# Kernel optimization log

Measured on AMD Instinct MI355X. Metric: run time of the kernel, lower is better.

Reference implementation:

```python
import jax, jax.numpy as jnp
import numpy as np

N = 10000
E = 160000
IN_CH = 128
HID = 128
HEADS = 4
OUT_CH = 1  # forced by nn.Linear(heads, 1) applied after conv2


def _linear_params(key, out_f, in_f):
    k1, k2 = jax.random.split(key)
    bound = 1.0 / np.sqrt(in_f)
    W = jax.random.uniform(k1, (out_f, in_f), jnp.float32, -bound, bound)
    b = jax.random.uniform(k2, (out_f,), jnp.float32, -bound, bound)
    return W, b


def setup_inputs() -> dict:
    key = jax.random.key(0)
    ks = jax.random.split(key, 12)
    x = jax.random.normal(ks[0], (N, IN_CH), jnp.float32)
    edge_index = jax.random.randint(ks[1], (2, E), 0, N, jnp.int64)

    # conv1: TransformerConv(IN_CH, HID, HEADS)
    Wq1, bq1 = _linear_params(ks[2], HEADS * HID, IN_CH)
    Wk1, bk1 = _linear_params(ks[3], HEADS * HID, IN_CH)
    Wv1, bv1 = _linear_params(ks[4], HEADS * HID, IN_CH)
    Ws1, bs1 = _linear_params(ks[5], HEADS * HID, IN_CH)  # root/skip

    # conv2: TransformerConv(HID*HEADS, OUT_CH, HEADS)
    d2 = HID * HEADS
    Wq2, bq2 = _linear_params(ks[6], HEADS * OUT_CH, d2)
    Wk2, bk2 = _linear_params(ks[7], HEADS * OUT_CH, d2)
    Wv2, bv2 = _linear_params(ks[8], HEADS * OUT_CH, d2)
    Ws2, bs2 = _linear_params(ks[9], HEADS * OUT_CH, d2)

    # final nn.Linear(HEADS, 1)
    Wl, bl = _linear_params(ks[10], 1, HEADS)

    return dict(x=x, edge_index=edge_index,
                Wq1=Wq1, bq1=bq1, Wk1=Wk1, bk1=bk1, Wv1=Wv1, bv1=bv1, Ws1=Ws1, bs1=bs1,
                Wq2=Wq2, bq2=bq2, Wk2=Wk2, bk2=bk2, Wv2=Wv2, bv2=bv2, Ws2=Ws2, bs2=bs2,
                Wl=Wl, bl=bl)


def transformer_conv(x, edge_index, Wq, bq, Wk, bk, Wv, bv, Ws, bs, heads, ch):
    # PyG TransformerConv defaults: concat=True, root_weight=True, beta=False
    n = x.shape[0]
    q = (x @ Wq.T + bq).reshape(n, heads, ch)
    k = (x @ Wk.T + bk).reshape(n, heads, ch)
    v = (x @ Wv.T + bv).reshape(n, heads, ch)

    src, dst = edge_index[0], edge_index[1]  # messages flow src -> dst
    # per-edge attention logits [E, H]
    logits = jnp.einsum('ehc,ehc->eh', q[dst], k[src]) / np.sqrt(ch).astype(np.float32)

    # segment softmax over edges grouped by destination node
    seg_max = jax.ops.segment_max(logits, dst, num_segments=n)  # [N, H]
    seg_max = jnp.where(jnp.isfinite(seg_max), seg_max, 0.0)
    ex = jnp.exp(logits - seg_max[dst])
    denom = jax.ops.segment_sum(ex, dst, num_segments=n)  # [N, H]
    alpha = ex / jnp.maximum(denom[dst], 1e-16)  # [E, H]

    # scatter-aggregate weighted values
    msgs = alpha[:, :, None] * v[src]  # [E, H, C]
    out = jax.ops.segment_sum(msgs, dst, num_segments=n)  # [N, H, C]
    out = out.reshape(n, heads * ch)
    # root/skip connection
    return out + (x @ Ws.T + bs)


def reference(x, edge_index,
              Wq1, bq1, Wk1, bk1, Wv1, bv1, Ws1, bs1,
              Wq2, bq2, Wk2, bk2, Wv2, bv2, Ws2, bs2,
              Wl, bl):
    h = transformer_conv(x, edge_index, Wq1, bq1, Wk1, bk1, Wv1, bv1, Ws1, bs1, HEADS, HID)
    h = jax.nn.relu(h)
    # dropout is identity in eval mode
    h = transformer_conv(h, edge_index, Wq2, bq2, Wk2, bk2, Wv2, bv2, Ws2, bs2, HEADS, OUT_CH)
    h = h @ Wl.T + bl  # [N, 1]
    return jnp.mean(h, axis=0, keepdims=True)  # [1, 1]
```

## Files before the change

kernel.cpp:

```cpp
#include <hip/hip_runtime.h>
#include <math.h>

#define NN 10000
#define NE 160000
#define NROWT 79
#define NGEMM (NROWT * 32)

typedef __attribute__((ext_vector_type(8))) short bf16x8;
typedef __attribute__((ext_vector_type(4))) float f32x4;
typedef __attribute__((ext_vector_type(2))) float f32x2;

#if defined(__has_builtin)
#if __has_builtin(__builtin_amdgcn_cvt_pk_fp8_f32) && __has_builtin(__builtin_amdgcn_cvt_pk_f32_fp8)
#define HW_FP8 1
#endif
#endif

__device__ inline ushort f2bf(float x) {
  uint u = __float_as_uint(x);
  return (ushort)((u + 0x7fffu + ((u >> 16) & 1u)) >> 16);
}

__device__ inline void unpack8(uint4 u, float* f) {
  f[0] = __uint_as_float(u.x << 16); f[1] = __uint_as_float(u.x & 0xffff0000u);
  f[2] = __uint_as_float(u.y << 16); f[3] = __uint_as_float(u.y & 0xffff0000u);
  f[4] = __uint_as_float(u.z << 16); f[5] = __uint_as_float(u.z & 0xffff0000u);
  f[6] = __uint_as_float(u.w << 16); f[7] = __uint_as_float(u.w & 0xffff0000u);
}

#ifndef HW_FP8
__device__ inline float fp8_dec1(uint b) {
  uint s = b >> 7, e = (b >> 3) & 15, m = b & 7;
  float v = (e == 0) ? ldexpf((float)m, -9) : ldexpf((float)(8 + m), (int)e - 10);
  return s ? -v : v;
}
__device__ inline uint fp8_enc1(float x) {
  uint s = (__float_as_uint(x) >> 31) << 7;
  float a = fabsf(x);
  if (!(a < 448.f)) return s | 0x7e;
  if (a < 9.765625e-4f) return s;
  int e; float m = frexpf(a, &e);
  int E = e - 1, q;
  if (E < -6) {
    q = (int)rintf(ldexpf(a, 9));
    if (q == 0) return s;
    if (q >= 8) return s | 8;
    return s | (uint)q;
  }
  q = (int)rintf(ldexpf(m, 4));
  if (q == 16) { q = 8; ++E; }
  if (E > 8 || (E == 8 && q == 15)) return s | 0x7e;
  return s | ((uint)(E + 7) << 3) | (uint)(q - 8);
}
#endif

__device__ inline uint pack4_fp8(float a, float b, float c, float d) {
#ifdef HW_FP8
  uint w = (uint)__builtin_amdgcn_cvt_pk_fp8_f32(a, b, 0, false);
  w = (uint)__builtin_amdgcn_cvt_pk_fp8_f32(c, d, (int)w, true);
  return w;
#else
  return fp8_enc1(a) | (fp8_enc1(b) << 8) | (fp8_enc1(c) << 16) | (fp8_enc1(d) << 24);
#endif
}

__device__ inline void dec8_fp8(uint2 u, float* f) {
#ifdef HW_FP8
  f32x2 p0 = __builtin_amdgcn_cvt_pk_f32_fp8((int)u.x, false);
  f32x2 p1 = __builtin_amdgcn_cvt_pk_f32_fp8((int)u.x, true);
  f32x2 p2 = __builtin_amdgcn_cvt_pk_f32_fp8((int)u.y, false);
  f32x2 p3 = __builtin_amdgcn_cvt_pk_f32_fp8((int)u.y, true);
  f[0] = p0.x; f[1] = p0.y; f[2] = p1.x; f[3] = p1.y;
  f[4] = p2.x; f[5] = p2.y; f[6] = p3.x; f[7] = p3.y;
#else
  f[0] = fp8_dec1(u.x & 255); f[1] = fp8_dec1((u.x >> 8) & 255);
  f[2] = fp8_dec1((u.x >> 16) & 255); f[3] = fp8_dec1(u.x >> 24);
  f[4] = fp8_dec1(u.y & 255); f[5] = fp8_dec1((u.y >> 8) & 255);
  f[6] = fp8_dec1((u.y >> 16) & 255); f[7] = fp8_dec1(u.y >> 24);
#endif
}

__global__ __launch_bounds__(256) void prep_k(
    const float* __restrict__ x,
    const float* __restrict__ Wq1, const float* __restrict__ Wk1,
    const float* __restrict__ Wv1, const float* __restrict__ Ws1,
    ushort* __restrict__ x_bf, ushort* __restrict__ w1bf,
    const int* __restrict__ dst, int* __restrict__ deg)
{
  int i = blockIdx.x * 256 + threadIdx.x;
  if (i < NE) atomicAdd(&deg[dst[i]], 1);
  const int n4x = NN * 32;
  const int n4w = 512 * 128 / 4;
  if (i < n4x) {
    float4 v = ((const float4*)x)[i];
    ushort4 o;
    o.x = f2bf(v.x); o.y = f2bf(v.y); o.z = f2bf(v.z); o.w = f2bf(v.w);
    ((ushort4*)x_bf)[i] = o;
  } else {
    int c = i - n4x;
    if (c < 4 * n4w) {
      int seg = c >> 14, k = c & 16383;
      const float* W = (seg == 0) ? Wq1 : (seg == 1) ? Wk1
                     : (seg == 2) ? Wv1 : Ws1;
      float4 v = ((const float4*)W)[k];
      ushort4 o;
      o.x = f2bf(v.x); o.y = f2bf(v.y); o.z = f2bf(v.z); o.w = f2bf(v.w);
      ((ushort4*)(w1bf + ((size_t)seg << 16)))[k] = o;
    }
  }
}

__global__ __launch_bounds__(1024) void scan_k(
    const int* __restrict__ deg, int* __restrict__ rowptr,
    int* __restrict__ cursor)
{
  __shared__ int part[1024];
  int tid = threadIdx.x;
  int base = tid * 10;
  int loc[10]; int s = 0;
  #pragma unroll
  for (int i = 0; i < 10; ++i) {
    int v = (base + i < NN) ? deg[base + i] : 0;
    loc[i] = s; s += v;
  }
  part[tid] = s;
  __syncthreads();
  for (int off = 1; off < 1024; off <<= 1) {
    int v = (tid >= off) ? part[tid - off] : 0;
    __syncthreads();
    part[tid] += v;
    __syncthreads();
  }
  int prev = (tid == 0) ? 0 : part[tid - 1];
  #pragma unroll
  for (int i = 0; i < 10; ++i) {
    int idx = base + i;
    if (idx < NN) { int r = prev + loc[i]; rowptr[idx] = r; cursor[idx] = r; }
  }
  if (tid == 1023) rowptr[NN] = part[1023];
}

__global__ __launch_bounds__(256) void gemm_scatter(
    const ushort* __restrict__ xbf, const ushort* __restrict__ wbf,
    const float* __restrict__ bq, const float* __restrict__ bk,
    const float* __restrict__ bv, const float* __restrict__ bs,
    ushort* __restrict__ qbf, unsigned char* __restrict__ k8,
    unsigned char* __restrict__ v8, float* __restrict__ h1,
    const int* __restrict__ src, const int* __restrict__ dst,
    int* __restrict__ cursor, int* __restrict__ csr_src)
{
  if (blockIdx.x >= NGEMM) {
    int e = (blockIdx.x - NGEMM) * 256 + threadIdx.x;
    if (e < NE) {
      int pos = atomicAdd(&cursor[dst[e]], 1);
      csr_src[pos] = src[e];
    }
    return;
  }
  __shared__ __align__(16) ushort Al[128 * 128];
  __shared__ __align__(16) ushort Bl[64 * 128];
  const int row0 = (blockIdx.x % NROWT) << 7;
  const int ncol0 = (blockIdx.x / NROWT) << 6;
  const int tid = threadIdx.x;

  #pragma unroll
  for (int i = 0; i < 8; ++i) {
    int slot = tid + (i << 8);
    int r = slot >> 4, c = slot & 15;
    int gr = row0 + r;
    uint4 v = make_uint4(0u, 0u, 0u, 0u);
    if (gr < NN) v = *(const uint4*)(xbf + (size_t)gr * 128 + (c << 3));
    *(uint4*)(Al + r * 128 + ((c ^ (r & 7)) << 3)) = v;
  }
  #pragma unroll
  for (int i = 0; i < 4; ++i) {
    int slot = tid + (i << 8);
    int r = slot >> 4, c = slot & 15;
    uint4 v = *(const uint4*)(wbf + (size_t)(ncol0 + r) * 128 + (c << 3));
    *(uint4*)(Bl + r * 128 + ((c ^ (r & 7)) << 3)) = v;
  }
  __syncthreads();

  const int wid = tid >> 6, lane = tid & 63;
  const int wm = wid >> 1, wn = wid & 1;
  const int lr = lane & 15, lkg = lane >> 4;
  const int seg = ncol0 >> 9;
  const int colInSeg = ncol0 & 511;
  const bool swp = (seg == 1) || (seg == 2);

  f32x4 acc[4][2];
  #pragma unroll
  for (int m = 0; m < 4; ++m)
    #pragma unroll
    for (int n = 0; n < 2; ++n) acc[m][n] = (f32x4){0.f, 0.f, 0.f, 0.f};

  #pragma unroll
  for (int ks = 0; ks < 4; ++ks) {
    int c16 = (ks << 2) + lkg;
    bf16x8 a[4], b[2];
    #pragma unroll
    for (int mf = 0; mf < 4; ++mf) {
      int r = (wm << 6) + (mf << 4) + lr;
      a[mf] = *(const bf16x8*)(Al + r * 128 + ((c16 ^ (r & 7)) << 3));
    }
    #pragma unroll
    for (int nf = 0; nf < 2; ++nf) {
      int r = (wn << 5) + (nf << 4) + lr;
      b[nf] = *(const bf16x8*)(Bl + r * 128 + ((c16 ^ (r & 7)) << 3));
    }
    if (swp) {
      #pragma unroll
      for (int mf = 0; mf < 4; ++mf)
        #pragma unroll
        for (int nf = 0; nf < 2; ++nf)
          acc[mf][nf] = __builtin_amdgcn_mfma_f32_16x16x32_bf16(
              b[nf], a[mf], acc[mf][nf], 0, 0, 0);
    } else {
      #pragma unroll
      for (int mf = 0; mf < 4; ++mf)
        #pragma unroll
        for (int nf = 0; nf < 2; ++nf)
          acc[mf][nf] = __builtin_amdgcn_mfma_f32_16x16x32_bf16(
              a[mf], b[nf], acc[mf][nf], 0, 0, 0);
    }
  }

  const float* bias = (seg == 0) ? bq : (seg == 1) ? bk : (seg == 2) ? bv : bs;
  if (swp) {
    unsigned char* out8 = (seg == 1) ? k8 : v8;
    #pragma unroll
    for (int mf = 0; mf < 4; ++mf) {
      int xrow = row0 + (wm << 6) + (mf << 4) + lr;
      if (xrow >= NN) continue;
      #pragma unroll
      for (int nf = 0; nf < 2; ++nf) {
        int ch = colInSeg + (wn << 5) + (nf << 4) + (lkg << 2);
        float4 bb = *(const float4*)(bias + ch);
        uint w = pack4_fp8(acc[mf][nf][0] + bb.x, acc[mf][nf][1] + bb.y,
                           acc[mf][nf][2] + bb.z, acc[mf][nf][3] + bb.w);
        *(uint*)(out8 + (size_t)xrow * 512 + ch) = w;
      }
    }
  } else {
    #pragma unroll
    for (int mf = 0; mf < 4; ++mf) {
      #pragma unroll
      for (int nf = 0; nf < 2; ++nf) {
        int col = colInSeg + (wn << 5) + (nf << 4) + lr;
        float bb = bias[col];
        #pragma unroll
        for (int r = 0; r < 4; ++r) {
          int row = row0 + (wm << 6) + (mf << 4) + (lkg << 2) + r;
          if (row >= NN) continue;
          float val = acc[mf][nf][r] + bb;
          if (seg == 0) qbf[(size_t)row * 512 + col] = f2bf(val);
          else          h1[(size_t)row * 512 + col] = val;
        }
      }
    }
  }
}

#define EDGE8(ku, vu)                                                      \
  {                                                                        \
    float kf[8], vf[8];                                                    \
    dec8_fp8(ku, kf); dec8_fp8(vu, vf);                                    \
    float t = q[0]*kf[0] + q[1]*kf[1] + q[2]*kf[2] + q[3]*kf[3]            \
            + q[4]*kf[4] + q[5]*kf[5] + q[6]*kf[6] + q[7]*kf[7];           \
    t += __shfl_xor(t, 1);                                                 \
    t += __shfl_xor(t, 2);                                                 \
    t += __shfl_xor(t, 4);                                                 \
    t += __shfl_xor(t, 8);                                                 \
    float ex = __expf(t);                                                  \
    den += ex;                                                             \
    _Pragma("unroll")                                                      \
    for (int i = 0; i < 8; ++i) acc[i] += ex * vf[i];                      \
  }

__global__ __launch_bounds__(256) void attn1(
    const ushort* __restrict__ qbf, const unsigned char* __restrict__ k8,
    const unsigned char* __restrict__ v8, const int* __restrict__ rowptr,
    const int* __restrict__ csr_src, float* __restrict__ h1)
{
  __shared__ float part[2][64][9];
  int slot = threadIdx.x >> 7;
  int sub = (threadIdx.x >> 6) & 1;
  int n = blockIdx.x * 2 + slot;
  int lane = threadIdx.x & 63;
  int h = lane >> 4, c0 = (lane & 15) << 3;
  const int off = h * 128 + c0;
  float q[8];
  unpack8(*(const uint4*)(qbf + (size_t)n * 512 + off), q);
  #pragma unroll
  for (int i = 0; i < 8; ++i) q[i] *= 0.08838834764831845f;
  float acc[8] = {};
  float den = 0.f;
  int j = rowptr[n] + sub * 2, e1 = rowptr[n + 1];
  for (; j + 1 < e1; j += 4) {
    int s0 = csr_src[j], s1 = csr_src[j + 1];
    uint2 ka = *(const uint2*)(k8 + (size_t)s0 * 512 + off);
    uint2 va = *(const uint2*)(v8 + (size_t)s0 * 512 + off);
    uint2 kb = *(const uint2*)(k8 + (size_t)s1 * 512 + off);
    uint2 vb = *(const uint2*)(v8 + (size_t)s1 * 512 + off);
    EDGE8(ka, va)
    EDGE8(kb, vb)
  }
  if (j < e1) {
    int s0 = csr_src[j];
    uint2 ka = *(const uint2*)(k8 + (size_t)s0 * 512 + off);
    uint2 va = *(const uint2*)(v8 + (size_t)s0 * 512 + off);
    EDGE8(ka, va)
  }
  if (sub == 1) {
    #pragma unroll
    for (int i = 0; i < 8; ++i) part[slot][lane][i] = acc[i];
    part[slot][lane][8] = den;
  }
  __syncthreads();
  if (sub == 0) {
    #pragma unroll
    for (int i = 0; i < 8; ++i) acc[i] += part[slot][lane][i];
    den += part[slot][lane][8];
    float inv = 1.f / fmaxf(den, 1e-16f);
    float* op = h1 + (size_t)n * 512 + off;
    float4 s0 = *(const float4*)op, s1 = *(const float4*)(op + 4);
    float4 o0, o1;
    o0.x = fmaxf(s0.x + acc[0] * inv, 0.f);
    o0.y = fmaxf(s0.y + acc[1] * inv, 0.f);
    o0.z = fmaxf(s0.z + acc[2] * inv, 0.f);
    o0.w = fmaxf(s0.w + acc[3] * inv, 0.f);
    o1.x = fmaxf(s1.x + acc[4] * inv, 0.f);
    o1.y = fmaxf(s1.y + acc[5] * inv, 0.f);
    o1.z = fmaxf(s1.z + acc[6] * inv, 0.f);
    o1.w = fmaxf(s1.w + acc[7] * inv, 0.f);
    *(float4*)op = o0;
    *(float4*)(op + 4) = o1;
  }
}

__global__ __launch_bounds__(256) void gemm_l2(
    const float* __restrict__ h1,
    const float* __restrict__ Wq, const float* __restrict__ bq,
    const float* __restrict__ Wk, const float* __restrict__ bk,
    const float* __restrict__ Wv, const float* __restrict__ bv,
    const float* __restrict__ Ws, const float* __restrict__ bs,
    float* __restrict__ qkv2, float* __restrict__ acc2)
{
  __shared__ float red[4][64][17];
  int n0 = blockIdx.x * 64;
  int wid = threadIdx.x >> 6, lane = threadIdx.x & 63;
  int n = n0 + lane;
  const float* Wm[4] = {Wq, Wk, Wv, Ws};
  float s[16] = {};
  if (n < NN) {
    const float* a = h1 + (size_t)n * 512 + wid * 128;
    #pragma unroll 4
    for (int i = 0; i < 128; i += 4) {
      float4 av = *(const float4*)(a + i);
      #pragma unroll
      for (int j = 0; j < 16; ++j) {
        const float* w = Wm[j >> 2] + (size_t)(j & 3) * 512 + wid * 128 + i;
        s[j] += av.x * w[0] + av.y * w[1] + av.z * w[2] + av.w * w[3];
      }
    }
  }
  #pragma unroll
  for (int j = 0; j < 16; ++j) red[wid][lane][j] = s[j];
  __syncthreads();
  #pragma unroll
  for (int q = 0; q < 4; ++q) {
    int idx = threadIdx.x * 4 + q;
    int ln = idx >> 4, j = idx & 15;
    int nn2 = n0 + ln;
    if (nn2 >= NN) continue;
    float v = red[0][ln][j] + red[1][ln][j] + red[2][ln][j] + red[3][ln][j];
    int sg = j >> 2, r = j & 3;
    const float* bb = (sg == 0) ? bq : (sg == 1) ? bk : (sg == 2) ? bv : bs;
    v += bb[r];
    if (sg < 3) qkv2[nn2 * 12 + sg * 4 + r] = v;
    else        acc2[nn2 * 4 + r] = v;
  }
}

__global__ __launch_bounds__(256) void attn2(
    const float* __restrict__ qkv2, const int* __restrict__ rowptr,
    const int* __restrict__ csr_src, float* __restrict__ acc2)
{
  int t = blockIdx.x * 256 + threadIdx.x;
  if (t >= NN * 16) return;
  int n = t >> 4, h = (t >> 2) & 3, part = t & 3;
  float q = qkv2[n * 12 + h];
  float den = 0.f, acc = 0.f;
  int e1 = rowptr[n + 1];
  for (int j = rowptr[n] + part; j < e1; j += 4) {
    int s = csr_src[j];
    float k = qkv2[s * 12 + 4 + h];
    float v = qkv2[s * 12 + 8 + h];
    float ex = __expf(q * k);
    den += ex; acc += ex * v;
  }
  den += __shfl_xor(den, 1); acc += __shfl_xor(acc, 1);
  den += __shfl_xor(den, 2); acc += __shfl_xor(acc, 2);
  if (part == 0) acc2[n * 4 + h] += acc / fmaxf(den, 1e-16f);
}

__global__ __launch_bounds__(1024) void final_k(
    const float* __restrict__ acc2, const float* __restrict__ Wl,
    const float* __restrict__ bl, float* __restrict__ out)
{
  __shared__ float red[1024];
  float w0 = Wl[0], w1 = Wl[1], w2 = Wl[2], w3 = Wl[3];
  float s = 0.f;
  for (int n = threadIdx.x; n < NN; n += 1024) {
    float4 a = ((const float4*)acc2)[n];
    s += a.x * w0 + a.y * w1 + a.z * w2 + a.w * w3;
  }
  red[threadIdx.x] = s;
  __syncthreads();
  for (int off = 512; off; off >>= 1) {
    if (threadIdx.x < off) red[threadIdx.x] += red[threadIdx.x + off];
    __syncthreads();
  }
  if (threadIdx.x == 0) out[0] = bl[0] + red[0] * (1.0f / NN);
}

extern "C" void kernel_launch(void* const* d_in, const int* in_sizes, int n_in,
                              void* d_out, int out_size, void* d_ws, size_t ws_size,
                              hipStream_t stream)
{
  const float* x   = (const float*)d_in[0];
  const int*   ei  = (const int*)d_in[1];
  const float *Wq1 = (const float*)d_in[2],  *bq1 = (const float*)d_in[3];
  const float *Wk1 = (const float*)d_in[4],  *bk1 = (const float*)d_in[5];
  const float *Wv1 = (const float*)d_in[6],  *bv1 = (const float*)d_in[7];
  const float *Ws1 = (const float*)d_in[8],  *bs1 = (const float*)d_in[9];
  const float *Wq2 = (const float*)d_in[10], *bq2 = (const float*)d_in[11];
  const float *Wk2 = (const float*)d_in[12], *bk2 = (const float*)d_in[13];
  const float *Wv2 = (const float*)d_in[14], *bv2 = (const float*)d_in[15];
  const float *Ws2 = (const float*)d_in[16], *bs2 = (const float*)d_in[17];
  const float *Wl  = (const float*)d_in[18], *bl  = (const float*)d_in[19];
  const int* srcp = ei;
  const int* dstp = ei + NE;

  ushort* qbf  = (ushort*)d_ws;
  ushort* x_bf = qbf + (size_t)NN * 512;
  ushort* w1bf = x_bf + (size_t)NN * 128;
  unsigned char* k8 = (unsigned char*)(w1bf + (size_t)2048 * 128);
  unsigned char* v8 = k8 + (size_t)NN * 512;
  float*  h1   = (float*)(v8 + (size_t)NN * 512);
  float*  qkv2 = h1 + (size_t)NN * 512;
  float*  acc2 = qkv2 + (size_t)NN * 12;
  int*   deg     = (int*)(acc2 + (size_t)NN * 4);
  int*   rowptr  = deg + NN;
  int*   cursor  = rowptr + NN + 1;
  int*   csr_src = cursor + NN;

  hipMemsetAsync(deg, 0, (size_t)NN * sizeof(int), stream);
  {
    const int total = NN * 32 + 4 * (512 * 128 / 4);
    prep_k<<<(total + 255) / 256, 256, 0, stream>>>(
        x, Wq1, Wk1, Wv1, Ws1, x_bf, w1bf, dstp, deg);
  }
  scan_k<<<1, 1024, 0, stream>>>(deg, rowptr, cursor);

  gemm_scatter<<<NGEMM + (NE + 255) / 256, 256, 0, stream>>>(
      x_bf, w1bf, bq1, bk1, bv1, bs1, qbf, k8, v8, h1,
      srcp, dstp, cursor, csr_src);

  attn1<<<NN / 2, 256, 0, stream>>>(qbf, k8, v8, rowptr, csr_src, h1);
  gemm_l2<<<(NN + 63) / 64, 256, 0, stream>>>(
      h1, Wq2, bq2, Wk2, bk2, Wv2, bv2, Ws2, bs2, qkv2, acc2);
  attn2<<<(NN * 16 + 255) / 256, 256, 0, stream>>>(qkv2, rowptr, csr_src, acc2);
  final_k<<<1, 1024, 0, stream>>>(acc2, Wl, bl, (float*)d_out);
}
```

Measured before the change: 135.5 us.

## Fuse attn2 with final reduction, widen attn1 to four waves per node

Merges the layer-2 attention kernel with the final mean reduction, using wave shuffles plus one atomic add per block, and replaces the memset with a small zero kernel that also clears the output. attn1 now gives each node a full block of four waves, each taking every fourth pair of edges, instead of two waves per node. This removes one launch and the single-block serial reduction, and adds parallelism to the edge gather. In exchange, the output is accumulated with float atomics, so the summation order is nondeterministic, and attn1 launches twice as many blocks.

```diff
diff --git a/kernel.cpp b/kernel.cpp
--- a/kernel.cpp
+++ b/kernel.cpp
@@ -78,6 +78,14 @@
   f[4] = fp8_dec1(u.y & 255); f[5] = fp8_dec1((u.y >> 8) & 255);
   f[6] = fp8_dec1((u.y >> 16) & 255); f[7] = fp8_dec1(u.y >> 24);
 #endif
+}
+
+__global__ __launch_bounds__(1024) void zero_k(
+    int* __restrict__ deg, float* __restrict__ out)
+{
+  int i = blockIdx.x * 1024 + threadIdx.x;
+  if (i < NN) deg[i] = 0;
+  if (i == 0) out[0] = 0.f;
 }
 
 __global__ __launch_bounds__(256) void prep_k(
@@ -282,10 +290,9 @@
     const unsigned char* __restrict__ v8, const int* __restrict__ rowptr,
     const int* __restrict__ csr_src, float* __restrict__ h1)
 {
-  __shared__ float part[2][64][9];
-  int slot = threadIdx.x >> 7;
-  int sub = (threadIdx.x >> 6) & 1;
-  int n = blockIdx.x * 2 + slot;
+  __shared__ float part[3][64][9];
+  int n = blockIdx.x;
+  int sub = threadIdx.x >> 6;
   int lane = threadIdx.x & 63;
   int h = lane >> 4, c0 = (lane & 15) << 3;
   const int off = h * 128 + c0;
@@ -295,8 +302,9 @@
   for (int i = 0; i < 8; ++i) q[i] *= 0.08838834764831845f;
   float acc[8] = {};
   float den = 0.f;
-  int j = rowptr[n] + sub * 2, e1 = rowptr[n + 1];
-  for (; j + 1 < e1; j += 4) {
+  int e1 = rowptr[n + 1];
+  int j = rowptr[n] + sub * 2;
+  for (; j + 1 < e1; j += 8) {
     int s0 = csr_src[j], s1 = csr_src[j + 1];
     uint2 ka = *(const uint2*)(k8 + (size_t)s0 * 512 + off);
     uint2 va = *(const uint2*)(v8 + (size_t)s0 * 512 + off);
@@ -311,16 +319,19 @@
     uint2 va = *(const uint2*)(v8 + (size_t)s0 * 512 + off);
     EDGE8(ka, va)
   }
-  if (sub == 1) {
-    #pragma unroll
-    for (int i = 0; i < 8; ++i) part[slot][lane][i] = acc[i];
-    part[slot][lane][8] = den;
+  if (sub > 0) {
+    #pragma unroll
+    for (int i = 0; i < 8; ++i) part[sub - 1][lane][i] = acc[i];
+    part[sub - 1][lane][8] = den;
   }
   __syncthreads();
   if (sub == 0) {
     #pragma unroll
-    for (int i = 0; i < 8; ++i) acc[i] += part[slot][lane][i];
-    den += part[slot][lane][8];
+    for (int w = 0; w < 3; ++w) {
+      #pragma unroll
+      for (int i = 0; i < 8; ++i) acc[i] += part[w][lane][i];
+      den += part[w][lane][8];
+    }
     float inv = 1.f / fmaxf(den, 1e-16f);
     float* op = h1 + (size_t)n * 512 + off;
     float4 s0 = *(const float4*)op, s1 = *(const float4*)(op + 4);
@@ -382,12 +393,14 @@
   }
 }
 
-__global__ __launch_bounds__(256) void attn2(
+__global__ __launch_bounds__(256) void attn2_final(
     const float* __restrict__ qkv2, const int* __restrict__ rowptr,
-    const int* __restrict__ csr_src, float* __restrict__ acc2)
-{
+    const int* __restrict__ csr_src, const float* __restrict__ acc2,
+    const float* __restrict__ Wl, const float* __restrict__ bl,
+    float* __restrict__ out)
+{
+  __shared__ float red[4];
   int t = blockIdx.x * 256 + threadIdx.x;
-  if (t >= NN * 16) return;
   int n = t >> 4, h = (t >> 2) & 3, part = t & 3;
   float q = qkv2[n * 12 + h];
   float den = 0.f, acc = 0.f;
@@ -401,27 +414,18 @@
   }
   den += __shfl_xor(den, 1); acc += __shfl_xor(acc, 1);
   den += __shfl_xor(den, 2); acc += __shfl_xor(acc, 2);
-  if (part == 0) acc2[n * 4 + h] += acc / fmaxf(den, 1e-16f);
-}
-
-__global__ __launch_bounds__(1024) void final_k(
-    const float* __restrict__ acc2, const float* __restrict__ Wl,
-    const float* __restrict__ bl, float* __restrict__ out)
-{
-  __shared__ float red[1024];
-  float w0 = Wl[0], w1 = Wl[1], w2 = Wl[2], w3 = Wl[3];
-  float s = 0.f;
-  for (int n = threadIdx.x; n < NN; n += 1024) {
-    float4 a = ((const float4*)acc2)[n];
-    s += a.x * w0 + a.y * w1 + a.z * w2 + a.w * w3;
-  }
-  red[threadIdx.x] = s;
+  float c = 0.f;
+  if (part == 0)
+    c = (acc2[n * 4 + h] + acc / fmaxf(den, 1e-16f)) * Wl[h] * (1.0f / NN);
+  if (t == 0) c += bl[0];
+  c += __shfl_xor(c, 4);
+  c += __shfl_xor(c, 8);
+  c += __shfl_xor(c, 16);
+  c += __shfl_xor(c, 32);
+  if ((threadIdx.x & 63) == 0) red[threadIdx.x >> 6] = c;
   __syncthreads();
-  for (int off = 512; off; off >>= 1) {
-    if (threadIdx.x < off) red[threadIdx.x] += red[threadIdx.x + off];
-    __syncthreads();
-  }
-  if (threadIdx.x == 0) out[0] = bl[0] + red[0] * (1.0f / NN);
+  if (threadIdx.x == 0)
+    unsafeAtomicAdd(out, red[0] + red[1] + red[2] + red[3]);
 }
 
 extern "C" void kernel_launch(void* const* d_in, const int* in_sizes, int n_in,
@@ -455,7 +459,7 @@
   int*   cursor  = rowptr + NN + 1;
   int*   csr_src = cursor + NN;
 
-  hipMemsetAsync(deg, 0, (size_t)NN * sizeof(int), stream);
+  zero_k<<<10, 1024, 0, stream>>>(deg, (float*)d_out);
   {
     const int total = NN * 32 + 4 * (512 * 128 / 4);
     prep_k<<<(total + 255) / 256, 256, 0, stream>>>(
@@ -467,9 +471,9 @@
       x_bf, w1bf, bq1, bk1, bv1, bs1, qbf, k8, v8, h1,
       srcp, dstp, cursor, csr_src);
 
-  attn1<<<NN / 2, 256, 0, stream>>>(qbf, k8, v8, rowptr, csr_src, h1);
+  attn1<<<NN, 256, 0, stream>>>(qbf, k8, v8, rowptr, csr_src, h1);
   gemm_l2<<<(NN + 63) / 64, 256, 0, stream>>>(
       h1, Wq2, bq2, Wk2, bk2, Wv2, bv2, Ws2, bs2, qkv2, acc2);
-  attn2<<<(NN * 16 + 255) / 256, 256, 0, stream>>>(qkv2, rowptr, csr_src, acc2);
-  final_k<<<1, 1024, 0, stream>>>(acc2, Wl, bl, (float*)d_out);
-}
+  attn2_final<<<NN * 16 / 256, 256, 0, stream>>>(
+      qkv2, rowptr, csr_src, acc2, Wl, bl, (float*)d_out);
+}
```

Result: no change. 136.9 us (+1.0%).
